# Kernel tuning notes

Hardware: AMD Instinct MI355X
Metric: run time of the kernel (lower is better)

The kernel has to match this reference:

```python
import jax, jax.numpy as jnp
import numpy as np

N = 100000      # nodes
E = 1600000     # edges (avg degree 16)
IN_DIM = 64
OUT_DIM = 128
BN_EPS = 1e-5


def setup_inputs() -> dict:
    key = jax.random.key(0)
    kx, ke, kw, kb, ks = jax.random.split(key, 5)
    x = jax.random.normal(kx, (N, IN_DIM), dtype=jnp.float32)
    edge_index = jax.random.randint(ke, (2, E), 0, N, dtype=jnp.int32)
    # GCNConv linear weight (no bias inside lin; conv bias separate)
    W = jax.random.normal(kw, (IN_DIM, OUT_DIM), dtype=jnp.float32) / np.sqrt(IN_DIM)
    bias = jax.random.normal(kb, (OUT_DIM,), dtype=jnp.float32) * 0.01
    # skip projection Linear(in_dim, out_dim, bias=False)
    skip_W = jax.random.normal(ks, (IN_DIM, OUT_DIM), dtype=jnp.float32) / np.sqrt(IN_DIM)
    # BatchNorm1d affine params (training-mode batch stats used in forward)
    gamma = jnp.ones((OUT_DIM,), dtype=jnp.float32)
    beta = jnp.zeros((OUT_DIM,), dtype=jnp.float32)
    return {"x": x, "edge_index": edge_index, "W": W, "bias": bias,
            "skip_W": skip_W, "gamma": gamma, "beta": beta}


def _gcn_forward(x, edge_index, W, bias, skip_W, gamma, beta):
    n = x.shape[0]
    # GCNConv, normalize=True, add_self_loops=True (PyG defaults)
    row, col = edge_index[0], edge_index[1]
    loop = jnp.arange(n, dtype=edge_index.dtype)
    row_f = jnp.concatenate([row, loop])   # source nodes
    col_f = jnp.concatenate([col, loop])   # target nodes

    xt = x @ W                             # [N, OUT]
    deg = jax.ops.segment_sum(jnp.ones_like(col_f, dtype=xt.dtype), col_f,
                              num_segments=n)          # >= 1 due to self loops
    dinv = jax.lax.rsqrt(deg)
    norm = dinv[row_f] * dinv[col_f]                    # [E+N]
    msgs = xt[row_f] * norm[:, None]                    # gather + scale
    out = jax.ops.segment_sum(msgs, col_f, num_segments=n) + bias

    # skip-sum (in_dim != out_dim -> project)
    out = out + x @ skip_W

    # BatchNorm1d (training-mode batch statistics), affine
    mean = out.mean(axis=0)
    var = out.var(axis=0)
    out = (out - mean) * jax.lax.rsqrt(var + BN_EPS) * gamma + beta

    # ReLU; dropout p=0.0 -> identity
    return jax.nn.relu(out)


def reference(x, edge_index, W, bias, skip_W, gamma, beta):
    return _gcn_forward(x, edge_index, W, bias, skip_W, gamma, beta)
```

## Files before the change

### kernel.cpp

```cpp
#include <hip/hip_runtime.h>


typedef unsigned short ushort;
typedef __bf16 bf16x8 __attribute__((ext_vector_type(8)));
typedef float f32x4 __attribute__((ext_vector_type(4)));
typedef float f32x2 __attribute__((ext_vector_type(2)));

constexpr int N_NODES = 100000;
constexpr int N_PAD   = 100096;
constexpr int E_EDGES = 1600000;

constexpr int BUCK_SHIFT = 7;
constexpr int NBUCK   = (N_NODES + 127) / 128;
constexpr int NBUCK_P = 784;
constexpr int CHUNK   = 8192;
constexpr int NCHUNK  = (E_EDGES + CHUNK - 1) / CHUNK;
constexpr int GH_STRIDE = 200;
constexpr int SORT_CAP = 4096;

constexpr size_t OFF_SCALE  = 0;
constexpr size_t OFF_DINV   = 256;
constexpr size_t OFF_ROWPTR = 100352;
constexpr size_t OFF_BASE   = 200480;
constexpr size_t OFF_GHIST  = 201280;
constexpr size_t OFF_BINNED = 358080;
constexpr size_t OFF_PART   = OFF_BINNED;
constexpr size_t OFF_U      = 1958080;
constexpr size_t OFF_PRE    = 5161152;
constexpr size_t OFF_XD8    = OFF_PRE;
constexpr size_t OFF_BT     = 11567296;

static __device__ __forceinline__ ushort f2bf(float f) {
    union { float f; unsigned u; } v; v.f = f;
    unsigned r = v.u + 0x7FFFu + ((v.u >> 16) & 1u);
    return (ushort)(r >> 16);
}
static __device__ __forceinline__ float bf2f(ushort u) {
    union { unsigned u; float f; } v; v.u = (unsigned)u << 16;
    return v.f;
}
static __device__ __forceinline__ unsigned pack_fp8x4(float a, float b, float c, float d) {
    int r = 0;
    r = __builtin_amdgcn_cvt_pk_fp8_f32(a, b, r, false);
    r = __builtin_amdgcn_cvt_pk_fp8_f32(c, d, r, true);
    return (unsigned)r;
}
static __device__ __forceinline__ bf16x8 pack_bf8(float4 a, float4 b) {
    union { ushort us[8]; bf16x8 v; } u;
    u.us[0] = f2bf(a.x); u.us[1] = f2bf(a.y); u.us[2] = f2bf(a.z); u.us[3] = f2bf(a.w);
    u.us[4] = f2bf(b.x); u.us[5] = f2bf(b.y); u.us[6] = f2bf(b.z); u.us[7] = f2bf(b.w);
    return u.v;
}

__global__ __launch_bounds__(256) void k_hist(const int* __restrict__ col,
                                              int* __restrict__ gh_t,
                                              const float* __restrict__ W,
                                              const float* __restrict__ skipW,
                                              ushort* __restrict__ Bt) {
    int c = blockIdx.x, t = threadIdx.x;
    if (c >= NCHUNK) {
        int idx = (c - NCHUNK) * 256 + t;
        int k = idx >> 7, n = idx & 127;
        float v = (k < 64) ? W[k * 128 + n] : skipW[(k - 64) * 128 + n];
        Bt[n * 128 + k] = f2bf(v);
        return;
    }
    __shared__ int h[NBUCK_P];
    for (int b = t; b < NBUCK_P; b += 256) h[b] = 0;
    __syncthreads();
    const int4* col4 = (const int4*)col;
    int g0 = c * (CHUNK / 4);
#pragma unroll
    for (int i = 0; i < CHUNK / 1024; ++i) {
        int g4 = g0 + i * 256 + t;
        if (g4 * 4 + 3 < E_EDGES) {
            int4 cc = col4[g4];
            atomicAdd(&h[cc.x >> BUCK_SHIFT], 1);
            atomicAdd(&h[cc.y >> BUCK_SHIFT], 1);
            atomicAdd(&h[cc.z >> BUCK_SHIFT], 1);
            atomicAdd(&h[cc.w >> BUCK_SHIFT], 1);
        } else {
#pragma unroll
            for (int j = 0; j < 4; ++j) {
                int e = g4 * 4 + j;
                if (e < E_EDGES) atomicAdd(&h[col[e] >> BUCK_SHIFT], 1);
            }
        }
    }
    __syncthreads();
    for (int b = t; b < NBUCK_P; b += 256) gh_t[(size_t)b * GH_STRIDE + c] = h[b];
}

__global__ __launch_bounds__(256) void k_scan_chunks(int* __restrict__ gh_t,
                                                     int* __restrict__ base) {
    int w = threadIdx.x >> 6, l = threadIdx.x & 63;
    int b = blockIdx.x * 4 + w;
    if (b >= NBUCK_P) return;
    int* rowp = gh_t + (size_t)b * GH_STRIDE;
    int carry = 0;
#pragma unroll
    for (int i = 0; i < 4; ++i) {
        int idx = i * 64 + l;
        int v = (idx < NCHUNK) ? rowp[idx] : 0;
        int orig = v;
#pragma unroll
        for (int d = 1; d < 64; d <<= 1) {
            int o = __shfl_up(v, d);
            if (l >= d) v += o;
        }
        if (idx < NCHUNK) rowp[idx] = carry + v - orig;
        carry += __shfl(v, 63);
    }
    if (l == 0 && b < NBUCK) base[b] = carry;
}

__global__ __launch_bounds__(1024) void k_scan_bases(int* __restrict__ base,
                                                     int* __restrict__ rowptr) {
    __shared__ int lds[1024];
    int t = threadIdx.x;
    int v = (t < NBUCK) ? base[t] : 0;
    lds[t] = v;
    __syncthreads();
    int val = v;
#pragma unroll
    for (int off = 1; off < 1024; off <<= 1) {
        int add = (t >= off) ? lds[t - off] : 0;
        __syncthreads();
        val += add;
        lds[t] = val;
        __syncthreads();
    }
    if (t < NBUCK) base[t] = val - v;
    if (t == 1023) {
        base[NBUCK] = val;
        rowptr[N_NODES] = val;
    }
}

__global__ __launch_bounds__(256) void k_scatter_bin(const int* __restrict__ row,
                                                     const int* __restrict__ col,
                                                     const int* __restrict__ gh_t,
                                                     const int* __restrict__ base,
                                                     unsigned int* __restrict__ binned) {
    __shared__ int cur[NBUCK_P];
    int c = blockIdx.x, t = threadIdx.x;
    for (int b = t; b < NBUCK_P; b += 256) {
        int bb = (b < NBUCK) ? base[b] : 0;
        cur[b] = bb + gh_t[(size_t)b * GH_STRIDE + c];
    }
    __syncthreads();
    const int4* col4 = (const int4*)col;
    const int4* row4 = (const int4*)row;
    int g0 = c * (CHUNK / 4);
#pragma unroll
    for (int i = 0; i < CHUNK / 1024; ++i) {
        int g4 = g0 + i * 256 + t;
        if (g4 * 4 + 3 < E_EDGES) {
            int4 cc = col4[g4];
            int4 rr = row4[g4];
            int p;
            p = atomicAdd(&cur[cc.x >> BUCK_SHIFT], 1);
            binned[p] = ((unsigned)(cc.x & 127) << 17) | (unsigned)rr.x;
            p = atomicAdd(&cur[cc.y >> BUCK_SHIFT], 1);
            binned[p] = ((unsigned)(cc.y & 127) << 17) | (unsigned)rr.y;
            p = atomicAdd(&cur[cc.z >> BUCK_SHIFT], 1);
            binned[p] = ((unsigned)(cc.z & 127) << 17) | (unsigned)rr.z;
            p = atomicAdd(&cur[cc.w >> BUCK_SHIFT], 1);
            binned[p] = ((unsigned)(cc.w & 127) << 17) | (unsigned)rr.w;
        } else {
#pragma unroll
            for (int j = 0; j < 4; ++j) {
                int e = g4 * 4 + j;
                if (e < E_EDGES) {
                    int d = col[e], s = row[e];
                    int p = atomicAdd(&cur[d >> BUCK_SHIFT], 1);
                    binned[p] = ((unsigned)(d & 127) << 17) | (unsigned)s;
                }
            }
        }
    }
}

__global__ __launch_bounds__(256) void k_sortbucket(unsigned int* __restrict__ binned,
                                                    const int* __restrict__ base,
                                                    int* __restrict__ rowptr,
                                                    float* __restrict__ dinv,
                                                    const float* __restrict__ x,
                                                    unsigned* __restrict__ xd8) {
    __shared__ unsigned int ebuf[SORT_CAP];
    __shared__ int sbuf[SORT_CAP];
    __shared__ int lcnt[128];
    __shared__ int lptr[128];
    __shared__ float ldinv[128];
    __shared__ int wsum[2];
    int b = blockIdx.x, t = threadIdx.x;
    int i0 = base[b], i1 = base[b + 1];
    int cnt = i1 - i0;
    if (cnt > SORT_CAP) cnt = SORT_CAP;
    int n0 = b << BUCK_SHIFT;
    int nn = min(128, N_NODES - n0);

    for (int k = t; k < cnt; k += 256) ebuf[k] = binned[i0 + k];
    if (t < 128) lcnt[t] = 0;
    __syncthreads();
    for (int k = t; k < cnt; k += 256) atomicAdd(&lcnt[ebuf[k] >> 17], 1);
    __syncthreads();

    int myc = 0, val = 0;
    if (t < 128) {
        myc = lcnt[t];
        val = myc;
#pragma unroll
        for (int d = 1; d < 64; d <<= 1) {
            int o = __shfl_up(val, d);
            if ((t & 63) >= d) val += o;
        }
        if ((t & 63) == 63) wsum[t >> 6] = val;
    }
    __syncthreads();
    if (t < 128) {
        if (t >= 64) val += wsum[0];
        int excl = val - myc;
        lptr[t] = excl;
        float dv = rsqrtf((float)myc + 1.0f);
        ldinv[t] = dv;
        if (t < nn) {
            rowptr[n0 + t] = i0 + excl;
            dinv[n0 + t] = dv;
        }
    }
    __syncthreads();
    for (int k = t; k < cnt; k += 256) {
        unsigned int e = ebuf[k];
        int j = (int)(e >> 17);
        int p = atomicAdd(&lptr[j], 1);
        sbuf[p] = (int)(e & 0x1FFFF);
    }
    __syncthreads();
    for (int k = t; k < cnt; k += 256) binned[i0 + k] = (unsigned int)sbuf[k];

#pragma unroll
    for (int it = 0; it < 8; ++it) {
        int idx = it * 256 + t;
        int nl = idx >> 4, q = idx & 15;
        int c = n0 + nl;
        unsigned w8 = 0;
        if (nl < nn) {
            float4 v = ((const float4*)x)[(size_t)c * 16 + q];
            float d = ldinv[nl];
            w8 = pack_fp8x4(v.x * d, v.y * d, v.z * d, v.w * d);
        }
        xd8[(size_t)c * 16 + q] = w8;
    }
}

__global__ __launch_bounds__(256) void k_agg(const unsigned* __restrict__ xd8,
                                             const float* __restrict__ dinv,
                                             const int* __restrict__ rowptr,
                                             const unsigned int* __restrict__ csr,
                                             ushort* __restrict__ u) {
    int t = blockIdx.x * blockDim.x + threadIdx.x;
    if (t >= N_PAD * 16) return;
    int c = t >> 4;
    int q = t & 15;
    if (c >= N_NODES) {
        ushort4 z = {0, 0, 0, 0};
        ((ushort4*)u)[t] = z;
        return;
    }
    float dc = dinv[c];
    float4 acc;
    {
        unsigned w = xd8[t];
        f32x2 lo = __builtin_amdgcn_cvt_pk_f32_fp8((int)w, false);
        f32x2 hi = __builtin_amdgcn_cvt_pk_f32_fp8((int)w, true);
        acc.x = lo.x; acc.y = lo.y; acc.z = hi.x; acc.w = hi.y;
    }
    int i0 = rowptr[c], i1 = rowptr[c + 1];
    int i = i0;
    for (; i + 8 <= i1; i += 8) {
        int s[8];
#pragma unroll
        for (int k = 0; k < 8; ++k) s[k] = (int)csr[i + k];
        unsigned w[8];
#pragma unroll
        for (int k = 0; k < 8; ++k) w[k] = xd8[s[k] * 16 + q];
#pragma unroll
        for (int k = 0; k < 8; ++k) {
            f32x2 lo = __builtin_amdgcn_cvt_pk_f32_fp8((int)w[k], false);
            f32x2 hi = __builtin_amdgcn_cvt_pk_f32_fp8((int)w[k], true);
            acc.x += lo.x; acc.y += lo.y; acc.z += hi.x; acc.w += hi.y;
        }
    }
    for (; i < i1; ++i) {
        unsigned w = xd8[(int)csr[i] * 16 + q];
        f32x2 lo = __builtin_amdgcn_cvt_pk_f32_fp8((int)w, false);
        f32x2 hi = __builtin_amdgcn_cvt_pk_f32_fp8((int)w, true);
        acc.x += lo.x; acc.y += lo.y; acc.z += hi.x; acc.w += hi.y;
    }
    ushort4 o;
    o.x = f2bf(acc.x * dc); o.y = f2bf(acc.y * dc);
    o.z = f2bf(acc.z * dc); o.w = f2bf(acc.w * dc);
    ((ushort4*)u)[t] = o;
}

__global__ __launch_bounds__(256) void k_gemm(const ushort* __restrict__ u,
                                              const float* __restrict__ x,
                                              const ushort* __restrict__ Bt,
                                              const float* __restrict__ bias,
                                              ushort* __restrict__ pre,
                                              float* __restrict__ partial) {
    __shared__ float sred[128];
    __shared__ float qred[128];
    int tid = threadIdx.x;
    int wave = tid >> 6, lane = tid & 63;
    int wm = wave >> 1, wn = wave & 1;
    int l15 = lane & 15, quad = lane >> 4;
    int row0 = blockIdx.x * 128 + wm * 64;
    int col0 = wn * 64;

    if (tid < 128) { sred[tid] = 0.f; qred[tid] = 0.f; }
    __syncthreads();

    bf16x8 af[4][4], bf_[4][4];
#pragma unroll
    for (int kc = 0; kc < 2; ++kc) {
        int ko = kc * 32 + quad * 8;
#pragma unroll
        for (int im = 0; im < 4; ++im)
            af[kc][im] = *(const bf16x8*)&u[(size_t)(row0 + im * 16 + l15) * 64 + ko];
    }
#pragma unroll
    for (int kc = 2; kc < 4; ++kc) {
        int ko = (kc - 2) * 32 + quad * 8;
#pragma unroll
        for (int im = 0; im < 4; ++im) {
            int r = row0 + im * 16 + l15;
            float4 v0 = make_float4(0.f, 0.f, 0.f, 0.f);
            float4 v1 = v0;
            if (r < N_NODES) {
                v0 = *(const float4*)&x[(size_t)r * 64 + ko];
                v1 = *(const float4*)&x[(size_t)r * 64 + ko + 4];
            }
            af[kc][im] = pack_bf8(v0, v1);
        }
    }
#pragma unroll
    for (int kc = 0; kc < 4; ++kc)
#pragma unroll
        for (int jn = 0; jn < 4; ++jn)
            bf_[kc][jn] = *(const bf16x8*)&Bt[(size_t)(col0 + jn * 16 + l15) * 128 + kc * 32 + quad * 8];

    f32x4 acc[4][4];
#pragma unroll
    for (int a = 0; a < 4; ++a)
#pragma unroll
        for (int b = 0; b < 4; ++b) acc[a][b] = (f32x4){0.f, 0.f, 0.f, 0.f};

#pragma unroll
    for (int kc = 0; kc < 4; ++kc)
#pragma unroll
        for (int im = 0; im < 4; ++im)
#pragma unroll
            for (int jn = 0; jn < 4; ++jn)
                acc[im][jn] = __builtin_amdgcn_mfma_f32_16x16x32_bf16(
                    af[kc][im], bf_[kc][jn], acc[im][jn], 0, 0, 0);

    int coln[4];
    float bi[4];
#pragma unroll
    for (int jn = 0; jn < 4; ++jn) {
        coln[jn] = col0 + jn * 16 + l15;
        bi[jn] = bias[coln[jn]];
    }
    float lsum[4] = {0.f, 0.f, 0.f, 0.f};
    float lsq[4]  = {0.f, 0.f, 0.f, 0.f};
#pragma unroll
    for (int im = 0; im < 4; ++im) {
        int rbase = row0 + im * 16 + quad * 4;
#pragma unroll
        for (int r = 0; r < 4; ++r) {
            int rowi = rbase + r;
            if (rowi < N_NODES) {
#pragma unroll
                for (int jn = 0; jn < 4; ++jn) {
                    float v = acc[im][jn][r] + bi[jn];
                    pre[(size_t)rowi * 128 + coln[jn]] = f2bf(v);
                    lsum[jn] += v;
                    lsq[jn]  += v * v;
                }
            }
        }
    }
#pragma unroll
    for (int jn = 0; jn < 4; ++jn) {
        atomicAdd(&sred[coln[jn]], lsum[jn]);
        atomicAdd(&qred[coln[jn]], lsq[jn]);
    }
    __syncthreads();
    if (tid < 128) {
        partial[(size_t)blockIdx.x * 256 + tid]       = sred[tid];
        partial[(size_t)blockIdx.x * 256 + 128 + tid] = qred[tid];
    }
}

__global__ __launch_bounds__(256) void k_reduce(const float* __restrict__ partial,
                                                const float* __restrict__ gamma,
                                                const float* __restrict__ beta,
                                                float* __restrict__ scaleshift) {
    __shared__ float ls[256], lq[256];
    int j = blockIdx.x;
    int t = threadIdx.x;
    float s = 0.f, q = 0.f;
    for (int p = t; p < NBUCK; p += 256) {
        s += partial[(size_t)p * 256 + j];
        q += partial[(size_t)p * 256 + 128 + j];
    }
    ls[t] = s; lq[t] = q;
    __syncthreads();
#pragma unroll
    for (int off = 128; off > 0; off >>= 1) {
        if (t < off) { ls[t] += ls[t + off]; lq[t] += lq[t + off]; }
        __syncthreads();
    }
    if (t == 0) {
        float mean = ls[0] * (1.0f / N_NODES);
        float var  = lq[0] * (1.0f / N_NODES) - mean * mean;
        float sc   = gamma[j] * rsqrtf(var + 1e-5f);
        scaleshift[j]       = sc;
        scaleshift[128 + j] = beta[j] - mean * sc;
    }
}

__global__ void k_apply(const ushort* __restrict__ pre, float* __restrict__ out,
                        const float* __restrict__ scaleshift) {
    int t = blockIdx.x * blockDim.x + threadIdx.x;
    if (t >= N_NODES * 32) return;
    int j4 = t & 31;
    ushort4 p = ((const ushort4*)pre)[t];
    float4 sc = ((const float4*)scaleshift)[j4];
    float4 sh = ((const float4*)(scaleshift + 128))[j4];
    float4 v;
    v.x = fmaxf(fmaf(bf2f(p.x), sc.x, sh.x), 0.f);
    v.y = fmaxf(fmaf(bf2f(p.y), sc.y, sh.y), 0.f);
    v.z = fmaxf(fmaf(bf2f(p.z), sc.z, sh.z), 0.f);
    v.w = fmaxf(fmaf(bf2f(p.w), sc.w, sh.w), 0.f);
    ((float4*)out)[t] = v;
}

extern "C" void kernel_launch(void* const* d_in, const int* in_sizes, int n_in,
                              void* d_out, int out_size, void* d_ws, size_t ws_size,
                              hipStream_t stream) {
    const float* x      = (const float*)d_in[0];
    const int*   eidx   = (const int*)d_in[1];
    const float* W      = (const float*)d_in[2];
    const float* bias   = (const float*)d_in[3];
    const float* skipW  = (const float*)d_in[4];
    const float* gamma  = (const float*)d_in[5];
    const float* beta   = (const float*)d_in[6];
    float* out = (float*)d_out;
    float* ws  = (float*)d_ws;

    const int* row = eidx;
    const int* col = eidx + E_EDGES;

    float* scaleshift = ws + OFF_SCALE;
    float* dinv       = ws + OFF_DINV;
    int*   rowptr     = (int*)(ws + OFF_ROWPTR);
    int*   base       = (int*)(ws + OFF_BASE);
    int*   gh_t       = (int*)(ws + OFF_GHIST);
    unsigned int* binned = (unsigned int*)(ws + OFF_BINNED);
    float* partial    = ws + OFF_PART;
    ushort* u         = (ushort*)(ws + OFF_U);
    unsigned* xd8     = (unsigned*)(ws + OFF_XD8);
    ushort* pre       = (ushort*)(ws + OFF_PRE);
    ushort* Bt        = (ushort*)(ws + OFF_BT);

    k_hist<<<NCHUNK + 64, 256, 0, stream>>>(col, gh_t, W, skipW, Bt);
    k_scan_chunks<<<(NBUCK_P + 3) / 4, 256, 0, stream>>>(gh_t, base);
    k_scan_bases<<<1, 1024, 0, stream>>>(base, rowptr);
    k_scatter_bin<<<NCHUNK, 256, 0, stream>>>(row, col, gh_t, base, binned);
    k_sortbucket<<<NBUCK, 256, 0, stream>>>(binned, base, rowptr, dinv, x, xd8);
    k_agg<<<(N_PAD * 16 + 255) / 256, 256, 0, stream>>>(xd8, dinv, rowptr, binned, u);
    k_gemm<<<NBUCK, 256, 0, stream>>>(u, x, Bt, bias, pre, partial);
    k_reduce<<<128, 256, 0, stream>>>(partial, gamma, beta, scaleshift);
    k_apply<<<(N_NODES * 32 + 255) / 256, 256, 0, stream>>>(pre, out, scaleshift);
}
```

Before: 205.8 us.

## Fuse scan and BN-stat reduction into last-block-done kernels, widen apply

Merges the two-kernel bucket scan into one kernel where the last block, found with an atomic ticket counter, performs the base prefix scan. It also folds the BatchNorm statistics reduction into the GEMM kernel using global float atomics and a last-block finalize, removing the partial buffer and a separate reduce launch. The apply kernel now processes eight bf16 values per thread. This saves two launches and their serialization gaps, but adds atomic contention, makes the float reduction order nondeterministic, and relies on correct memory ordering for the ticket pattern.

```diff
diff --git a/kernel.cpp b/kernel.cpp
--- a/kernel.cpp
+++ b/kernel.cpp
@@ -5,6 +5,7 @@
 typedef __bf16 bf16x8 __attribute__((ext_vector_type(8)));
 typedef float f32x4 __attribute__((ext_vector_type(4)));
 typedef float f32x2 __attribute__((ext_vector_type(2)));
+typedef ushort u16x8 __attribute__((ext_vector_type(8)));
 
 constexpr int N_NODES = 100000;
 constexpr int N_PAD   = 100096;
@@ -24,11 +25,12 @@
 constexpr size_t OFF_BASE   = 200480;
 constexpr size_t OFF_GHIST  = 201280;
 constexpr size_t OFF_BINNED = 358080;
-constexpr size_t OFF_PART   = OFF_BINNED;
 constexpr size_t OFF_U      = 1958080;
 constexpr size_t OFF_PRE    = 5161152;
 constexpr size_t OFF_XD8    = OFF_PRE;
 constexpr size_t OFF_BT     = 11567296;
+constexpr size_t OFF_GSUM   = 11575488;
+constexpr size_t OFF_TICK   = 11575744;
 
 static __device__ __forceinline__ ushort f2bf(float f) {
     union { float f; unsigned u; } v; v.f = f;
@@ -56,10 +58,16 @@
                                               int* __restrict__ gh_t,
                                               const float* __restrict__ W,
                                               const float* __restrict__ skipW,
-                                              ushort* __restrict__ Bt) {
+                                              ushort* __restrict__ Bt,
+                                              float* __restrict__ gsum,
+                                              unsigned* __restrict__ tick) {
     int c = blockIdx.x, t = threadIdx.x;
     if (c >= NCHUNK) {
         int idx = (c - NCHUNK) * 256 + t;
+        if (c == NCHUNK) {
+            gsum[t] = 0.f;
+            if (t < 2) tick[t] = 0u;
+        }
         int k = idx >> 7, n = idx & 127;
         float v = (k < 64) ? W[k * 128 + n] : skipW[(k - 64) * 128 + n];
         Bt[n * 128 + k] = f2bf(v);
@@ -91,11 +99,14 @@
     for (int b = t; b < NBUCK_P; b += 256) gh_t[(size_t)b * GH_STRIDE + c] = h[b];
 }
 
-__global__ __launch_bounds__(256) void k_scan_chunks(int* __restrict__ gh_t,
-                                                     int* __restrict__ base) {
+__global__ __launch_bounds__(256) void k_scan(int* __restrict__ gh_t,
+                                              int* __restrict__ base,
+                                              int* __restrict__ rowptr,
+                                              unsigned* __restrict__ tick) {
+    __shared__ int wtot[4];
+    __shared__ int amlast;
     int w = threadIdx.x >> 6, l = threadIdx.x & 63;
     int b = blockIdx.x * 4 + w;
-    if (b >= NBUCK_P) return;
     int* rowp = gh_t + (size_t)b * GH_STRIDE;
     int carry = 0;
 #pragma unroll
@@ -111,29 +122,39 @@
         if (idx < NCHUNK) rowp[idx] = carry + v - orig;
         carry += __shfl(v, 63);
     }
-    if (l == 0 && b < NBUCK) base[b] = carry;
-}
-
-__global__ __launch_bounds__(1024) void k_scan_bases(int* __restrict__ base,
-                                                     int* __restrict__ rowptr) {
-    __shared__ int lds[1024];
+    if (l == 0 && b < NBUCK) atomicExch(&base[b], carry);
+    __syncthreads();
+    if (threadIdx.x == 0)
+        amlast = (atomicAdd(tick + 0, 1u) == (unsigned)(gridDim.x - 1)) ? 1 : 0;
+    __syncthreads();
+    if (!amlast) return;
+
     int t = threadIdx.x;
-    int v = (t < NBUCK) ? base[t] : 0;
-    lds[t] = v;
-    __syncthreads();
-    int val = v;
-#pragma unroll
-    for (int off = 1; off < 1024; off <<= 1) {
-        int add = (t >= off) ? lds[t - off] : 0;
-        __syncthreads();
-        val += add;
-        lds[t] = val;
-        __syncthreads();
-    }
-    if (t < NBUCK) base[t] = val - v;
-    if (t == 1023) {
-        base[NBUCK] = val;
-        rowptr[N_NODES] = val;
+    int i0 = t * 4;
+    int v0 = (i0 + 0 < NBUCK) ? atomicAdd(&base[i0 + 0], 0) : 0;
+    int v1 = (i0 + 1 < NBUCK) ? atomicAdd(&base[i0 + 1], 0) : 0;
+    int v2 = (i0 + 2 < NBUCK) ? atomicAdd(&base[i0 + 2], 0) : 0;
+    int v3 = (i0 + 3 < NBUCK) ? atomicAdd(&base[i0 + 3], 0) : 0;
+    int s = v0 + v1 + v2 + v3;
+    int incl = s;
+#pragma unroll
+    for (int d = 1; d < 64; d <<= 1) {
+        int o = __shfl_up(incl, d);
+        if (l >= d) incl += o;
+    }
+    if (l == 63) wtot[w] = incl;
+    __syncthreads();
+    int wpre = 0;
+    for (int ww = 0; ww < w; ++ww) wpre += wtot[ww];
+    int excl = wpre + incl - s;
+    if (i0 + 0 < NBUCK) base[i0 + 0] = excl;
+    if (i0 + 1 < NBUCK) base[i0 + 1] = excl + v0;
+    if (i0 + 2 < NBUCK) base[i0 + 2] = excl + v0 + v1;
+    if (i0 + 3 < NBUCK) base[i0 + 3] = excl + v0 + v1 + v2;
+    if (t == 255) {
+        int total = wpre + incl;
+        base[NBUCK] = total;
+        rowptr[N_NODES] = total;
     }
 }
 
@@ -309,9 +330,14 @@
                                               const ushort* __restrict__ Bt,
                                               const float* __restrict__ bias,
                                               ushort* __restrict__ pre,
-                                              float* __restrict__ partial) {
+                                              float* __restrict__ gsum,
+                                              unsigned* __restrict__ tick,
+                                              const float* __restrict__ gamma,
+                                              const float* __restrict__ beta,
+                                              float* __restrict__ scaleshift) {
     __shared__ float sred[128];
     __shared__ float qred[128];
+    __shared__ int amlast;
     int tid = threadIdx.x;
     int wave = tid >> 6, lane = tid & 63;
     int wm = wave >> 1, wn = wave & 1;
@@ -399,53 +425,46 @@
     }
     __syncthreads();
     if (tid < 128) {
-        partial[(size_t)blockIdx.x * 256 + tid]       = sred[tid];
-        partial[(size_t)blockIdx.x * 256 + 128 + tid] = qred[tid];
-    }
-}
-
-__global__ __launch_bounds__(256) void k_reduce(const float* __restrict__ partial,
-                                                const float* __restrict__ gamma,
-                                                const float* __restrict__ beta,
-                                                float* __restrict__ scaleshift) {
-    __shared__ float ls[256], lq[256];
-    int j = blockIdx.x;
-    int t = threadIdx.x;
-    float s = 0.f, q = 0.f;
-    for (int p = t; p < NBUCK; p += 256) {
-        s += partial[(size_t)p * 256 + j];
-        q += partial[(size_t)p * 256 + 128 + j];
-    }
-    ls[t] = s; lq[t] = q;
-    __syncthreads();
-#pragma unroll
-    for (int off = 128; off > 0; off >>= 1) {
-        if (t < off) { ls[t] += ls[t + off]; lq[t] += lq[t + off]; }
-        __syncthreads();
-    }
-    if (t == 0) {
-        float mean = ls[0] * (1.0f / N_NODES);
-        float var  = lq[0] * (1.0f / N_NODES) - mean * mean;
-        float sc   = gamma[j] * rsqrtf(var + 1e-5f);
-        scaleshift[j]       = sc;
-        scaleshift[128 + j] = beta[j] - mean * sc;
-    }
-}
-
-__global__ void k_apply(const ushort* __restrict__ pre, float* __restrict__ out,
-                        const float* __restrict__ scaleshift) {
+        atomicAdd(&gsum[tid], sred[tid]);
+        atomicAdd(&gsum[128 + tid], qred[tid]);
+    }
+    __syncthreads();
+    if (tid == 0)
+        amlast = (atomicAdd(tick + 1, 1u) == (unsigned)(gridDim.x - 1)) ? 1 : 0;
+    __syncthreads();
+    if (amlast && tid < 128) {
+        float s = atomicAdd(&gsum[tid], 0.f);
+        float q = atomicAdd(&gsum[128 + tid], 0.f);
+        float mean = s * (1.0f / N_NODES);
+        float var  = q * (1.0f / N_NODES) - mean * mean;
+        float sc   = gamma[tid] * rsqrtf(var + 1e-5f);
+        scaleshift[tid]       = sc;
+        scaleshift[128 + tid] = beta[tid] - mean * sc;
+    }
+}
+
+__global__ __launch_bounds__(256) void k_apply(const ushort* __restrict__ pre,
+                                               float* __restrict__ out,
+                                               const float* __restrict__ ss) {
     int t = blockIdx.x * blockDim.x + threadIdx.x;
-    if (t >= N_NODES * 32) return;
-    int j4 = t & 31;
-    ushort4 p = ((const ushort4*)pre)[t];
-    float4 sc = ((const float4*)scaleshift)[j4];
-    float4 sh = ((const float4*)(scaleshift + 128))[j4];
-    float4 v;
-    v.x = fmaxf(fmaf(bf2f(p.x), sc.x, sh.x), 0.f);
-    v.y = fmaxf(fmaf(bf2f(p.y), sc.y, sh.y), 0.f);
-    v.z = fmaxf(fmaf(bf2f(p.z), sc.z, sh.z), 0.f);
-    v.w = fmaxf(fmaf(bf2f(p.w), sc.w, sh.w), 0.f);
-    ((float4*)out)[t] = v;
+    if (t >= N_NODES * 16) return;
+    int j8 = t & 15;
+    u16x8 p = ((const u16x8*)pre)[t];
+    float4 sc0 = ((const float4*)ss)[j8 * 2];
+    float4 sc1 = ((const float4*)ss)[j8 * 2 + 1];
+    float4 sh0 = ((const float4*)(ss + 128))[j8 * 2];
+    float4 sh1 = ((const float4*)(ss + 128))[j8 * 2 + 1];
+    float4 v0, v1;
+    v0.x = fmaxf(fmaf(bf2f(p[0]), sc0.x, sh0.x), 0.f);
+    v0.y = fmaxf(fmaf(bf2f(p[1]), sc0.y, sh0.y), 0.f);
+    v0.z = fmaxf(fmaf(bf2f(p[2]), sc0.z, sh0.z), 0.f);
+    v0.w = fmaxf(fmaf(bf2f(p[3]), sc0.w, sh0.w), 0.f);
+    v1.x = fmaxf(fmaf(bf2f(p[4]), sc1.x, sh1.x), 0.f);
+    v1.y = fmaxf(fmaf(bf2f(p[5]), sc1.y, sh1.y), 0.f);
+    v1.z = fmaxf(fmaf(bf2f(p[6]), sc1.z, sh1.z), 0.f);
+    v1.w = fmaxf(fmaf(bf2f(p[7]), sc1.w, sh1.w), 0.f);
+    ((float4*)out)[t * 2]     = v0;
+    ((float4*)out)[t * 2 + 1] = v1;
 }
 
 extern "C" void kernel_launch(void* const* d_in, const int* in_sizes, int n_in,
@@ -470,19 +489,18 @@
     int*   base       = (int*)(ws + OFF_BASE);
     int*   gh_t       = (int*)(ws + OFF_GHIST);
     unsigned int* binned = (unsigned int*)(ws + OFF_BINNED);
-    float* partial    = ws + OFF_PART;
     ushort* u         = (ushort*)(ws + OFF_U);
     unsigned* xd8     = (unsigned*)(ws + OFF_XD8);
     ushort* pre       = (ushort*)(ws + OFF_PRE);
     ushort* Bt        = (ushort*)(ws + OFF_BT);
-
-    k_hist<<<NCHUNK + 64, 256, 0, stream>>>(col, gh_t, W, skipW, Bt);
-    k_scan_chunks<<<(NBUCK_P + 3) / 4, 256, 0, stream>>>(gh_t, base);
-    k_scan_bases<<<1, 1024, 0, stream>>>(base, rowptr);
+    float* gsum       = ws + OFF_GSUM;
+    unsigned* tick    = (unsigned*)(ws + OFF_TICK);
+
+    k_hist<<<NCHUNK + 64, 256, 0, stream>>>(col, gh_t, W, skipW, Bt, gsum, tick);
+    k_scan<<<NBUCK_P / 4, 256, 0, stream>>>(gh_t, base, rowptr, tick);
     k_scatter_bin<<<NCHUNK, 256, 0, stream>>>(row, col, gh_t, base, binned);
     k_sortbucket<<<NBUCK, 256, 0, stream>>>(binned, base, rowptr, dinv, x, xd8);
     k_agg<<<(N_PAD * 16 + 255) / 256, 256, 0, stream>>>(xd8, dinv, rowptr, binned, u);
-    k_gemm<<<NBUCK, 256, 0, stream>>>(u, x, Bt, bias, pre, partial);
-    k_reduce<<<128, 256, 0, stream>>>(partial, gamma, beta, scaleshift);
-    k_apply<<<(N_NODES * 32 + 255) / 256, 256, 0, stream>>>(pre, out, scaleshift);
-}
+    k_gemm<<<NBUCK, 256, 0, stream>>>(u, x, Bt, bias, pre, gsum, tick, gamma, beta, scaleshift);
+    k_apply<<<(N_NODES * 16 + 255) / 256, 256, 0, stream>>>(pre, out, scaleshift);
+}
```

Measured after the change: 217.2 us. 5.5% more time.
